# Performance work log

Hardware: AMD Instinct MI355X
Metric: run time of the kernel (lower is better)

The kernel has to match this reference:

```python
import jax, jax.numpy as jnp
import numpy as np
from jax import lax

B, P, C = 2, 512, 5                 # images, proposals/img, classes (incl. background)
IN_FEAT, REP = 12544, 1024          # 256*7*7 pooled features; TwoMLPHead width
H_IMG = W_IMG = 800.0
SCORE_THRESH, NMS_THRESH, DET_PER_IMG = 0.05, 0.5, 100
MIN_SIZE = 0.01
WX, WY, WW, WH = 10.0, 10.0, 5.0, 5.0
BBOX_CLIP = float(np.log(1000.0 / 16.0))
NEG = -1e9


def _make_boxes(key, n):
    k1, k2, k3, k4 = jax.random.split(key, 4)
    cx = jax.random.uniform(k1, (n,)) * W_IMG
    cy = jax.random.uniform(k2, (n,)) * H_IMG
    bw = jax.random.uniform(k3, (n,)) * 180.0 + 20.0
    bh = jax.random.uniform(k4, (n,)) * 180.0 + 20.0
    x1 = jnp.clip(cx - bw / 2, 0.0, W_IMG)
    y1 = jnp.clip(cy - bh / 2, 0.0, H_IMG)
    x2 = jnp.clip(cx + bw / 2, 0.0, W_IMG)
    y2 = jnp.clip(cy + bh / 2, 0.0, H_IMG)
    return jnp.stack([x1, y1, x2, y2], -1).astype(jnp.float32)


def setup_inputs() -> dict:
    ks = jax.random.split(jax.random.key(0), 12)
    box_features = jax.random.normal(ks[0], (B * P, IN_FEAT), jnp.float32)
    proposals = jnp.stack([_make_boxes(ks[1 + i], P) for i in range(B)])
    def w(k, shp):
        return (jax.random.normal(k, shp, jnp.float32) / np.sqrt(shp[0])).astype(jnp.float32)
    return {
        'box_features': box_features,
        'proposals': proposals,
        'W1': w(ks[3], (IN_FEAT, REP)), 'b1': jnp.zeros((REP,), jnp.float32),
        'W2': w(ks[4], (REP, REP)),     'b2': jnp.zeros((REP,), jnp.float32),
        'Wc': w(ks[5], (REP, C)),       'bc': jnp.zeros((C,), jnp.float32),
        'Wb': w(ks[6], (REP, 4 * C)),   'bb': jnp.zeros((4 * C,), jnp.float32),
    }


def box_iou(a, b):
    area_a = (a[:, 2] - a[:, 0]) * (a[:, 3] - a[:, 1])
    area_b = (b[:, 2] - b[:, 0]) * (b[:, 3] - b[:, 1])
    lt = jnp.maximum(a[:, None, :2], b[None, :, :2])
    rb = jnp.minimum(a[:, None, 2:], b[None, :, 2:])
    wh = jnp.clip(rb - lt, 0.0)
    inter = wh[..., 0] * wh[..., 1]
    return inter / (area_a[:, None] + area_b[None, :] - inter + 1e-9)


def decode(reg, props):
    # reg: [N, C, 4] raw deltas; props: [N, 4] xyxy  (torchvision BoxCoder.decode)
    w = props[:, 2] - props[:, 0]
    h = props[:, 3] - props[:, 1]
    cx = props[:, 0] + 0.5 * w
    cy = props[:, 1] + 0.5 * h
    dx, dy = reg[..., 0] / WX, reg[..., 1] / WY
    dw = jnp.minimum(reg[..., 2] / WW, BBOX_CLIP)
    dh = jnp.minimum(reg[..., 3] / WH, BBOX_CLIP)
    pcx = dx * w[:, None] + cx[:, None]
    pcy = dy * h[:, None] + cy[:, None]
    pw = jnp.exp(dw) * w[:, None]
    ph = jnp.exp(dh) * h[:, None]
    return jnp.stack([pcx - 0.5 * pw, pcy - 0.5 * ph, pcx + 0.5 * pw, pcy + 0.5 * ph], -1)


def postprocess_one(boxes, scores, labels):
    # boxes [M,4] (already clipped), scores [M], labels [M] int; fixed-size output.
    M = boxes.shape[0]
    ws = boxes[:, 2] - boxes[:, 0]
    hs = boxes[:, 3] - boxes[:, 1]
    valid = (scores > SCORE_THRESH) & (ws >= MIN_SIZE) & (hs >= MIN_SIZE)
    order = jnp.argsort(-scores)
    b, s, l, v = boxes[order], scores[order], labels[order], valid[order]
    # batched (per-class) NMS via class-offset trick
    off = l.astype(b.dtype)[:, None] * (max(H_IMG, W_IMG) + 1.0)
    iou = box_iou(b + off, b + off)
    idxs = jnp.arange(M)

    def body(i, keep):
        sup = (iou[i] > NMS_THRESH) & keep[i] & (idxs > i)
        return keep & ~sup

    keep = lax.fori_loop(0, M, body, v)
    sc = jnp.where(keep, s, NEG)
    top_s, top_i = lax.top_k(sc, DET_PER_IMG)
    ok = top_s > NEG / 2
    tb = jnp.where(ok[:, None], b[top_i], 0.0)
    tl = jnp.where(ok, l[top_i], 0)
    ts = jnp.where(ok, top_s, 0.0)
    return tb, ts, tl


def reference(box_features, proposals, W1, b1, W2, b2, Wc, bc, Wb, bb):
    # box_head: TwoMLPHead
    h = jax.nn.relu(box_features @ W1 + b1)
    h = jax.nn.relu(h @ W2 + b2)
    # box_predictor
    class_logits = h @ Wc + bc                       # [N, C]
    box_regression = (h @ Wb + bb).reshape(-1, C, 4)  # [N, C, 4]
    props = proposals.reshape(-1, 4)
    pred = decode(box_regression, props)             # [N, C, 4]
    # clip to image
    pred = jnp.stack([
        jnp.clip(pred[..., 0], 0.0, W_IMG), jnp.clip(pred[..., 1], 0.0, H_IMG),
        jnp.clip(pred[..., 2], 0.0, W_IMG), jnp.clip(pred[..., 3], 0.0, H_IMG)], -1)
    scores = jax.nn.softmax(class_logits, -1)        # [N, C]
    # drop background class, flatten proposal-major (matches torch reshape(-1,4))
    pb = pred[:, 1:, :].reshape(B, P * (C - 1), 4)
    sc = scores[:, 1:].reshape(B, P * (C - 1))
    labels = jnp.tile(jnp.arange(1, C, dtype=jnp.int32), P)  # [M]
    boxes_o, scores_o, labels_o = jax.vmap(postprocess_one, in_axes=(0, 0, None))(pb, sc, labels)
    return boxes_o, scores_o, labels_o
```

## Files before the change

kernel.cpp:

```cpp
#include <hip/hip_runtime.h>
#include <math.h>

#define NROWS 1024
#define K1    12544
#define REP   1024
#define NDET  2048
#define DETS  100
#define BBOX_CLIP_F 4.135166556742356f

typedef __attribute__((ext_vector_type(8))) short bf16x8;
typedef __attribute__((ext_vector_type(4))) float f32x4;

__device__ __forceinline__ unsigned short rne_bf16(float x) {
  unsigned u = __float_as_uint(x);
  u += 0x7fffu + ((u >> 16) & 1u);
  return (unsigned short)(u >> 16);
}
__device__ __forceinline__ float bf16f(unsigned short h) {
  return __uint_as_float(((unsigned)h) << 16);
}
__device__ __forceinline__ int swz(int r, int s) {
  return s ^ (r & 3) ^ ((r >> 2) & 3);
}
__device__ __forceinline__ void gload16(const void* g, void* lds) {
  __builtin_amdgcn_global_load_lds(
      (const __attribute__((address_space(1))) unsigned int*)g,
      (__attribute__((address_space(3))) unsigned int*)lds, 16, 0, 0);
}

__global__ __launch_bounds__(256) void pack_fused(
    const float* __restrict__ X, const float* __restrict__ W1,
    const float* __restrict__ W2, const float* __restrict__ Wc,
    const float* __restrict__ Wb,
    unsigned short* __restrict__ Ahp, unsigned short* __restrict__ Alp,
    unsigned short* __restrict__ W1h, unsigned short* __restrict__ W1l,
    unsigned short* __restrict__ W2h, unsigned short* __restrict__ W2l,
    float* __restrict__ Wt) {
  __shared__ unsigned short th[32 * 36], tl[32 * 36];
  const int id = blockIdx.x;
  const int t = threadIdx.x;
  if (id < 13568) {
    const float* W;
    unsigned short *Oh, *Ol;
    int nKB, kb, n0;
    if (id < 12544) { W = W1; Oh = W1h; Ol = W1l; nKB = 392; kb = id % 392; n0 = (id / 392) * 32; }
    else { const int r2 = id - 12544; W = W2; Oh = W2h; Ol = W2l; nKB = 32; kb = r2 % 32; n0 = (r2 / 32) * 32; }
    const int r = t >> 3, c4 = (t & 7) << 2;
    float4 v = *(const float4*)&W[(size_t)(kb * 32 + r) * REP + n0 + c4];
    float fv[4] = {v.x, v.y, v.z, v.w};
#pragma unroll
    for (int j = 0; j < 4; ++j) {
      unsigned short h = rne_bf16(fv[j]);
      th[(c4 + j) * 36 + r] = h;
      tl[(c4 + j) * 36 + r] = rne_bf16(fv[j] - bf16f(h));
    }
    __syncthreads();
    const int half = t >> 7;
    const int n_loc = (t & 127) >> 2, slot = t & 3;
    const unsigned short* src = (half ? tl : th) + n_loc * 36 + slot * 8;
    ushort4 u0 = *(const ushort4*)src;
    ushort4 u1 = *(const ushort4*)(src + 4);
    const int n = n0 + n_loc, rb = n >> 7, rr = n & 127;
    size_t chunk = ((size_t)(rb * nKB + kb)) * 512 + rr * 4 + swz(rr, slot);
    unsigned short* dst = (half ? Ol : Oh) + chunk * 8;
    *(ushort4*)dst = u0;
    *(ushort4*)(dst + 4) = u1;
  } else if (id < 19840) {
    const int r_ = id - 13568;
    const int kb = r_ % 392;
    const int row = (r_ / 392) * 64 + (t >> 2);
    const int slot = t & 3;
    const float* p = X + (size_t)row * K1 + kb * 32 + slot * 8;
    float4 f0 = *(const float4*)p;
    float4 f1 = *(const float4*)(p + 4);
    float fv[8] = {f0.x, f0.y, f0.z, f0.w, f1.x, f1.y, f1.z, f1.w};
    unsigned short hh[8], ll[8];
#pragma unroll
    for (int j = 0; j < 8; ++j) {
      hh[j] = rne_bf16(fv[j]);
      ll[j] = rne_bf16(fv[j] - bf16f(hh[j]));
    }
    const int rb = row >> 7, rr = row & 127;
    size_t chunk = ((size_t)(rb * 392 + kb)) * 512 + rr * 4 + swz(rr, slot);
    unsigned short* dh = Ahp + chunk * 8;
    unsigned short* dl = Alp + chunk * 8;
    *(ushort4*)dh = make_ushort4(hh[0], hh[1], hh[2], hh[3]);
    *(ushort4*)(dh + 4) = make_ushort4(hh[4], hh[5], hh[6], hh[7]);
    *(ushort4*)dl = make_ushort4(ll[0], ll[1], ll[2], ll[3]);
    *(ushort4*)(dl + 4) = make_ushort4(ll[4], ll[5], ll[6], ll[7]);
  } else {
    const int i = (id - 19840) * 256 + t;
    if (i < 25 * 1024) {
      const int o = i >> 10, k = i & 1023;
      Wt[i] = (o < 5) ? Wc[(size_t)k * 5 + o] : Wb[(size_t)k * 20 + (o - 5)];
    }
  }
}

__global__ __launch_bounds__(256) void pack_b(
    const float* __restrict__ W, unsigned short* __restrict__ Oh,
    unsigned short* __restrict__ Ol, int nKB) {
  __shared__ unsigned short th[32 * 36], tl[32 * 36];
  const int kb = blockIdx.x, n0 = blockIdx.y * 32;
  const int t = threadIdx.x;
  const int r = t >> 3, c4 = (t & 7) << 2;
  float4 v = *(const float4*)&W[(size_t)(kb * 32 + r) * REP + n0 + c4];
  float fv[4] = {v.x, v.y, v.z, v.w};
#pragma unroll
  for (int j = 0; j < 4; ++j) {
    unsigned short h = rne_bf16(fv[j]);
    th[(c4 + j) * 36 + r] = h;
    tl[(c4 + j) * 36 + r] = rne_bf16(fv[j] - bf16f(h));
  }
  __syncthreads();
  const int half = t >> 7;
  const int n_loc = (t & 127) >> 2, slot = t & 3;
  const unsigned short* src = (half ? tl : th) + n_loc * 36 + slot * 8;
  ushort4 u0 = *(const ushort4*)src;
  ushort4 u1 = *(const ushort4*)(src + 4);
  const int n = n0 + n_loc, rb = n >> 7, rr = n & 127;
  size_t chunk = ((size_t)(rb * nKB + kb)) * 512 + rr * 4 + swz(rr, slot);
  unsigned short* dst = (half ? Ol : Oh) + chunk * 8;
  *(ushort4*)dst = u0;
  *(ushort4*)(dst + 4) = u1;
}

__global__ __launch_bounds__(256) void gemm_pk2(
    const unsigned short* __restrict__ Ah, const unsigned short* __restrict__ Al,
    const unsigned short* __restrict__ Bh, const unsigned short* __restrict__ Bl,
    float* __restrict__ T, int nKB, int stepsPerZ) {
  __shared__ __align__(16) unsigned short lds[2][4][4096];
  const int tid = threadIdx.x;
  const int w = tid >> 6, l = tid & 63;
  const int r_ = blockIdx.x, t_ = blockIdx.y;
  const int rbA = (r_ & 3) * 2 + (t_ & 1);
  const int rbB = (r_ >> 2) * 4 + (t_ >> 1);
  const int tk0 = blockIdx.z * stepsPerZ;
  const int fr = l & 15, q = l >> 4;
  const int wr = (w >> 1) * 64, wc = (w & 1) * 64;
  const int qs = q ^ (fr & 3) ^ (fr >> 2);
  const int aoff = ((wr + fr) * 4 + qs) * 16;
  const int boff = ((wc + fr) * 4 + qs) * 16;

  auto stage = [&](int bf, int tk) {
    const unsigned short* ga_h = Ah + ((size_t)(rbA * nKB + tk)) * 4096;
    const unsigned short* ga_l = Al + ((size_t)(rbA * nKB + tk)) * 4096;
    const unsigned short* gb_h = Bh + ((size_t)(rbB * nKB + tk)) * 4096;
    const unsigned short* gb_l = Bl + ((size_t)(rbB * nKB + tk)) * 4096;
#pragma unroll
    for (int rseg = 0; rseg < 2; ++rseg) {
      const int seg = rseg * 4 + w;
      const size_t go = (size_t)(seg * 64 + l) * 8;
      gload16(ga_h + go, &lds[bf][0][seg * 512]);
      gload16(ga_l + go, &lds[bf][1][seg * 512]);
      gload16(gb_h + go, &lds[bf][2][seg * 512]);
      gload16(gb_l + go, &lds[bf][3][seg * 512]);
    }
  };

  f32x4 acc[4][4];
#pragma unroll
  for (int m = 0; m < 4; ++m)
#pragma unroll
    for (int n = 0; n < 4; ++n) acc[m][n] = (f32x4){0.f, 0.f, 0.f, 0.f};

  stage(0, tk0);
  if (stepsPerZ > 1) {
    stage(1, tk0 + 1);
    asm volatile("s_waitcnt vmcnt(8)");
  } else {
    asm volatile("s_waitcnt vmcnt(0)");
  }
  __builtin_amdgcn_s_barrier();
  __builtin_amdgcn_sched_barrier(0);

  int cur = 0;
  for (int s = 0; s < stepsPerZ; ++s) {
    const char* La  = (const char*)&lds[cur][0][0];
    const char* Ll  = (const char*)&lds[cur][1][0];
    const char* Lbh = (const char*)&lds[cur][2][0];
    const char* Lbl = (const char*)&lds[cur][3][0];
    bf16x8 ah[4], al[4], bh[4], bl[4];
#pragma unroll
    for (int m = 0; m < 4; ++m) {
      ah[m] = *(const bf16x8*)(La + aoff + m * 1024);
      al[m] = *(const bf16x8*)(Ll + aoff + m * 1024);
    }
#pragma unroll
    for (int n = 0; n < 4; ++n) {
      bh[n] = *(const bf16x8*)(Lbh + boff + n * 1024);
      bl[n] = *(const bf16x8*)(Lbl + boff + n * 1024);
    }
#pragma unroll
    for (int m = 0; m < 4; ++m)
#pragma unroll
      for (int n = 0; n < 4; ++n) {
        acc[m][n] = __builtin_amdgcn_mfma_f32_16x16x32_bf16(ah[m], bh[n], acc[m][n], 0, 0, 0);
        acc[m][n] = __builtin_amdgcn_mfma_f32_16x16x32_bf16(ah[m], bl[n], acc[m][n], 0, 0, 0);
        acc[m][n] = __builtin_amdgcn_mfma_f32_16x16x32_bf16(al[m], bh[n], acc[m][n], 0, 0, 0);
      }
    if (s + 1 < stepsPerZ) {
      __builtin_amdgcn_s_barrier();
      if (s + 2 < stepsPerZ) {
        stage(cur, tk0 + s + 2);
        asm volatile("s_waitcnt vmcnt(8)");
      } else {
        asm volatile("s_waitcnt vmcnt(0)");
      }
      __builtin_amdgcn_s_barrier();
      __builtin_amdgcn_sched_barrier(0);
    }
    cur ^= 1;
  }
  float* Tz = T + (size_t)blockIdx.z * (NROWS * REP);
#pragma unroll
  for (int m = 0; m < 4; ++m) {
    const int r0 = rbA * 128 + wr + m * 16 + ((l >> 4) << 2);
#pragma unroll
    for (int n = 0; n < 4; ++n) {
      const int c = rbB * 128 + wc + n * 16 + fr;
#pragma unroll
      for (int j = 0; j < 4; ++j) Tz[(size_t)(r0 + j) * REP + c] = acc[m][n][j];
    }
  }
}

__global__ __launch_bounds__(256) void combine8_relu_pack(
    const float* __restrict__ T, const float* __restrict__ bias,
    unsigned short* __restrict__ Oh, unsigned short* __restrict__ Ol) {
  const int e = (blockIdx.x * 256 + threadIdx.x) * 8;
  const int MN = NROWS * REP;
  float s[8];
  {
    float4 a0 = *(const float4*)&T[e];
    float4 a1 = *(const float4*)&T[e + 4];
    s[0] = a0.x; s[1] = a0.y; s[2] = a0.z; s[3] = a0.w;
    s[4] = a1.x; s[5] = a1.y; s[6] = a1.z; s[7] = a1.w;
  }
#pragma unroll
  for (int z = 1; z < 8; ++z) {
    float4 a0 = *(const float4*)&T[z * MN + e];
    float4 a1 = *(const float4*)&T[z * MN + e + 4];
    s[0] += a0.x; s[1] += a0.y; s[2] += a0.z; s[3] += a0.w;
    s[4] += a1.x; s[5] += a1.y; s[6] += a1.z; s[7] += a1.w;
  }
  const int c0 = e & 1023;
  float4 b0 = *(const float4*)&bias[c0];
  float4 b1 = *(const float4*)&bias[c0 + 4];
  s[0] = fmaxf(s[0] + b0.x, 0.f); s[1] = fmaxf(s[1] + b0.y, 0.f);
  s[2] = fmaxf(s[2] + b0.z, 0.f); s[3] = fmaxf(s[3] + b0.w, 0.f);
  s[4] = fmaxf(s[4] + b1.x, 0.f); s[5] = fmaxf(s[5] + b1.y, 0.f);
  s[6] = fmaxf(s[6] + b1.z, 0.f); s[7] = fmaxf(s[7] + b1.w, 0.f);
  unsigned short hh[8], ll[8];
#pragma unroll
  for (int j = 0; j < 8; ++j) {
    hh[j] = rne_bf16(s[j]);
    ll[j] = rne_bf16(s[j] - bf16f(hh[j]));
  }
  const int r = e >> 10;
  const int kb = c0 >> 5, slot = (c0 >> 3) & 3;
  const int rb = r >> 7, rr = r & 127;
  size_t chunk = ((size_t)(rb * 32 + kb)) * 512 + rr * 4 + swz(rr, slot);
  unsigned short* dh = Oh + chunk * 8;
  unsigned short* dl = Ol + chunk * 8;
  *(ushort4*)dh = make_ushort4(hh[0], hh[1], hh[2], hh[3]);
  *(ushort4*)(dh + 4) = make_ushort4(hh[4], hh[5], hh[6], hh[7]);
  *(ushort4*)dl = make_ushort4(ll[0], ll[1], ll[2], ll[3]);
  *(ushort4*)(dl + 4) = make_ushort4(ll[4], ll[5], ll[6], ll[7]);
}

__global__ __launch_bounds__(256) void combineN_relu(
    const float* __restrict__ T, const float* __restrict__ bias,
    float* __restrict__ H, int nz) {
  const int i = blockIdx.x * 256 + threadIdx.x;
  const int MN4 = NROWS * REP / 4;
  const float4* t = (const float4*)T;
  float4 s0 = t[i];
  for (int z = 1; z < nz; ++z) {
    float4 v = t[i + z * MN4];
    s0.x += v.x; s0.y += v.y; s0.z += v.z; s0.w += v.w;
  }
  float4 bs = ((const float4*)bias)[i & 255];
  float4 r;
  r.x = fmaxf(s0.x + bs.x, 0.f);
  r.y = fmaxf(s0.y + bs.y, 0.f);
  r.z = fmaxf(s0.z + bs.z, 0.f);
  r.w = fmaxf(s0.w + bs.w, 0.f);
  ((float4*)H)[i] = r;
}

__global__ __launch_bounds__(256) void gemm_pk(
    const float* __restrict__ A, const unsigned short* __restrict__ Bh,
    const unsigned short* __restrict__ Bl, float* __restrict__ T,
    int K, int nKB, int stepsPerZ) {
  __shared__ __align__(16) unsigned short lds[2][4][4096];
  const int tid = threadIdx.x;
  const int w = tid >> 6, l = tid & 63;
  const int bm = blockIdx.x * 128;
  const int bnb = blockIdx.y;
  const int tk0 = blockIdx.z * stepsPerZ;
  const int arow = tid >> 1, ahalf = tid & 1;
  const int fr = l & 15, q = l >> 4;
  const int wr = (w >> 1) * 64, wc = (w & 1) * 64;
  const int qs = q ^ (fr & 3) ^ (fr >> 2);
  const int aoff = ((wr + fr) * 4 + qs) * 16;
  const int boff = ((wc + fr) * 4 + qs) * 16;
  const float* aptr = A + (size_t)(bm + arow) * K + ahalf * 16;

  float4 av[4];
  auto loadA = [&](int tk) {
    const float* p = aptr + tk * 32;
#pragma unroll
    for (int j = 0; j < 4; ++j) av[j] = *(const float4*)(p + j * 4);
  };
  auto stageB = [&](int bf, int tk) {
    const unsigned short* gh = Bh + ((size_t)(bnb * nKB + tk)) * 4096;
    const unsigned short* gl_ = Bl + ((size_t)(bnb * nKB + tk)) * 4096;
#pragma unroll
    for (int rseg = 0; rseg < 2; ++rseg) {
      const int seg = rseg * 4 + w;
      gload16(gh + (size_t)(seg * 64 + l) * 8, &lds[bf][2][seg * 512]);
      gload16(gl_ + (size_t)(seg * 64 + l) * 8, &lds[bf][3][seg * 512]);
    }
  };
  auto writeA = [&](int bf) {
#pragma unroll
    for (int j = 0; j < 2; ++j) {
      const int s_ = ahalf * 2 + j;
      float fv[8] = {av[j * 2].x, av[j * 2].y, av[j * 2].z, av[j * 2].w,
                     av[j * 2 + 1].x, av[j * 2 + 1].y, av[j * 2 + 1].z, av[j * 2 + 1].w};
      unsigned hp[4], lp[4];
#pragma unroll
      for (int p2 = 0; p2 < 4; ++p2) {
        unsigned short h0 = rne_bf16(fv[2 * p2]), h1 = rne_bf16(fv[2 * p2 + 1]);
        float l0 = fv[2 * p2] - bf16f(h0), l1 = fv[2 * p2 + 1] - bf16f(h1);
        hp[p2] = (unsigned)h0 | ((unsigned)h1 << 16);
        lp[p2] = (unsigned)rne_bf16(l0) | ((unsigned)rne_bf16(l1) << 16);
      }
      const int chunk = arow * 4 + swz(arow, s_);
      *(uint4*)&lds[bf][0][chunk * 8] = make_uint4(hp[0], hp[1], hp[2], hp[3]);
      *(uint4*)&lds[bf][1][chunk * 8] = make_uint4(lp[0], lp[1], lp[2], lp[3]);
    }
  };

  f32x4 acc[4][4];
#pragma unroll
  for (int m = 0; m < 4; ++m)
#pragma unroll
    for (int n = 0; n < 4; ++n) acc[m][n] = (f32x4){0.f, 0.f, 0.f, 0.f};

  loadA(tk0);
  stageB(0, tk0);
  writeA(0);
  __syncthreads();
  int cur = 0;
  for (int s = 0; s < stepsPerZ; ++s) {
    const bool nx = (s + 1 < stepsPerZ);
    if (nx) { loadA(tk0 + s + 1); stageB(cur ^ 1, tk0 + s + 1); }
    const char* La = (const char*)&lds[cur][0][0];
    const char* Ll = (const char*)&lds[cur][1][0];
    const char* Lbh = (const char*)&lds[cur][2][0];
    const char* Lbl = (const char*)&lds[cur][3][0];
    bf16x8 ah[4], al[4], bh[4], bl[4];
#pragma unroll
    for (int m = 0; m < 4; ++m) {
      ah[m] = *(const bf16x8*)(La + aoff + m * 1024);
      al[m] = *(const bf16x8*)(Ll + aoff + m * 1024);
    }
#pragma unroll
    for (int n = 0; n < 4; ++n) {
      bh[n] = *(const bf16x8*)(Lbh + boff + n * 1024);
      bl[n] = *(const bf16x8*)(Lbl + boff + n * 1024);
    }
#pragma unroll
    for (int m = 0; m < 4; ++m)
#pragma unroll
      for (int n = 0; n < 4; ++n) {
        acc[m][n] = __builtin_amdgcn_mfma_f32_16x16x32_bf16(ah[m], bh[n], acc[m][n], 0, 0, 0);
        acc[m][n] = __builtin_amdgcn_mfma_f32_16x16x32_bf16(ah[m], bl[n], acc[m][n], 0, 0, 0);
        acc[m][n] = __builtin_amdgcn_mfma_f32_16x16x32_bf16(al[m], bh[n], acc[m][n], 0, 0, 0);
      }
    if (nx) writeA(cur ^ 1);
    __syncthreads();
    cur ^= 1;
  }
  float* Tz = T + (size_t)blockIdx.z * (NROWS * REP);
#pragma unroll
  for (int m = 0; m < 4; ++m) {
    const int r0 = bm + wr + m * 16 + ((l >> 4) << 2);
#pragma unroll
    for (int n = 0; n < 4; ++n) {
      const int c = bnb * 128 + wc + n * 16 + fr;
#pragma unroll
      for (int j = 0; j < 4; ++j) Tz[(size_t)(r0 + j) * REP + c] = acc[m][n][j];
    }
  }
}

__global__ __launch_bounds__(256) void gemm64(
    const float* __restrict__ A, const float* __restrict__ W,
    float* __restrict__ T, int K, int N, int kChunk) {
  __shared__ float As[32][68];
  __shared__ float Bs[32][64];
  const int tid = threadIdx.x;
  const int bm = blockIdx.x * 64, bn = blockIdx.y * 64;
  const int k0 = blockIdx.z * kChunk;
  const int tx = tid & 15, ty = tid >> 4;
  const int ar = tid >> 3;
  const int ac = (tid & 7) << 2;
  const int br = tid >> 4;
  const int bc = (tid & 15) << 2;
  float acc[4][4] = {{0.f,0.f,0.f,0.f},{0.f,0.f,0.f,0.f},{0.f,0.f,0.f,0.f},{0.f,0.f,0.f,0.f}};
  for (int kk = k0; kk < k0 + kChunk; kk += 32) {
    float4 a0 = *(const float4*)&A[(size_t)(bm + ar) * K + kk + ac];
    float4 a1 = *(const float4*)&A[(size_t)(bm + ar + 32) * K + kk + ac];
    float4 b0 = *(const float4*)&W[(size_t)(kk + br) * N + bn + bc];
    float4 b1 = *(const float4*)&W[(size_t)(kk + br + 16) * N + bn + bc];
    As[ac+0][ar] = a0.x; As[ac+1][ar] = a0.y; As[ac+2][ar] = a0.z; As[ac+3][ar] = a0.w;
    As[ac+0][ar+32] = a1.x; As[ac+1][ar+32] = a1.y; As[ac+2][ar+32] = a1.z; As[ac+3][ar+32] = a1.w;
    *(float4*)&Bs[br][bc]    = b0;
    *(float4*)&Bs[br+16][bc] = b1;
    __syncthreads();
#pragma unroll
    for (int k = 0; k < 32; ++k) {
      float4 av = *(const float4*)&As[k][ty << 2];
      float4 bv = *(const float4*)&Bs[k][tx << 2];
      float a_[4] = {av.x, av.y, av.z, av.w};
      float b_[4] = {bv.x, bv.y, bv.z, bv.w};
#pragma unroll
      for (int i = 0; i < 4; ++i)
#pragma unroll
        for (int j = 0; j < 4; ++j)
          acc[i][j] = fmaf(a_[i], b_[j], acc[i][j]);
    }
    __syncthreads();
  }
  float* Tz = T + (size_t)blockIdx.z * NROWS * REP;
#pragma unroll
  for (int i = 0; i < 4; ++i) {
    float4 v = make_float4(acc[i][0], acc[i][1], acc[i][2], acc[i][3]);
    *(float4*)&Tz[(size_t)(bm + (ty << 2) + i) * N + bn + (tx << 2)] = v;
  }
}

__global__ __launch_bounds__(256) void heads2(
    const float* __restrict__ H2, const float* __restrict__ Wt,
    const float* __restrict__ bcv, const float* __restrict__ bbv,
    const float* __restrict__ props, float* __restrict__ pb, float* __restrict__ sc) {
  const int wave = threadIdx.x >> 6, l = threadIdx.x & 63;
  const int n = blockIdx.x * 4 + wave;
  const float* h = H2 + (size_t)n * REP + l * 16;
  float4 h0 = *(const float4*)h, h1 = *(const float4*)(h + 4);
  float4 h2v = *(const float4*)(h + 8), h3 = *(const float4*)(h + 12);
  float outv[25];
#pragma unroll
  for (int o = 0; o < 25; ++o) {
    const float* wp = Wt + o * REP + l * 16;
    float4 w0 = *(const float4*)wp, w1 = *(const float4*)(wp + 4);
    float4 w2 = *(const float4*)(wp + 8), w3 = *(const float4*)(wp + 12);
    float d = h0.x * w0.x;
    d = fmaf(h0.y, w0.y, d); d = fmaf(h0.z, w0.z, d); d = fmaf(h0.w, w0.w, d);
    d = fmaf(h1.x, w1.x, d); d = fmaf(h1.y, w1.y, d); d = fmaf(h1.z, w1.z, d); d = fmaf(h1.w, w1.w, d);
    d = fmaf(h2v.x, w2.x, d); d = fmaf(h2v.y, w2.y, d); d = fmaf(h2v.z, w2.z, d); d = fmaf(h2v.w, w2.w, d);
    d = fmaf(h3.x, w3.x, d); d = fmaf(h3.y, w3.y, d); d = fmaf(h3.z, w3.z, d); d = fmaf(h3.w, w3.w, d);
#pragma unroll
    for (int m = 1; m < 64; m <<= 1) d += __shfl_xor(d, m);
    outv[o] = d + ((o < 5) ? bcv[o] : bbv[o - 5]);
  }
  const float mx = fmaxf(fmaxf(fmaxf(outv[0], outv[1]), fmaxf(outv[2], outv[3])), outv[4]);
  const float e0 = expf(outv[0] - mx), e1 = expf(outv[1] - mx), e2 = expf(outv[2] - mx);
  const float e3 = expf(outv[3] - mx), e4 = expf(outv[4] - mx);
  const float inv = 1.0f / (e0 + e1 + e2 + e3 + e4);
  const float s1 = e1 * inv, s2 = e2 * inv, s3 = e3 * inv, s4 = e4 * inv;
  const float* pr = props + (size_t)n * 4;
  const float x1 = pr[0], y1 = pr[1], x2 = pr[2], y2 = pr[3];
  const float bw = x2 - x1, bh = y2 - y1;
  const float cx = x1 + 0.5f * bw, cy = y1 + 0.5f * bh;
  const int img = n >> 9, pbase = (n & 511) << 2;
#pragma unroll
  for (int c = 1; c <= 4; ++c) {
    if (l == c - 1) {
      const float r0 = outv[5 + c * 4 + 0], r1 = outv[5 + c * 4 + 1];
      const float r2 = outv[5 + c * 4 + 2], r3 = outv[5 + c * 4 + 3];
      const float dx = r0 / 10.0f, dy = r1 / 10.0f;
      const float dw = fminf(r2 / 5.0f, BBOX_CLIP_F);
      const float dh = fminf(r3 / 5.0f, BBOX_CLIP_F);
      const float pcx = dx * bw + cx, pcy = dy * bh + cy;
      const float pw = expf(dw) * bw, ph = expf(dh) * bh;
      float bx1 = pcx - 0.5f * pw, by1 = pcy - 0.5f * ph;
      float bx2 = pcx + 0.5f * pw, by2 = pcy + 0.5f * ph;
      bx1 = fminf(fmaxf(bx1, 0.f), 800.f);
      by1 = fminf(fmaxf(by1, 0.f), 800.f);
      bx2 = fminf(fmaxf(bx2, 0.f), 800.f);
      by2 = fminf(fmaxf(by2, 0.f), 800.f);
      const int pidx = pbase + (c - 1);
      float* o = pb + (size_t)(img * NDET + pidx) * 4;
      o[0] = bx1; o[1] = by1; o[2] = bx2; o[3] = by2;
      const float smc = (c == 1) ? s1 : (c == 2) ? s2 : (c == 3) ? s3 : s4;
      sc[img * NDET + pidx] = smc;
    }
  }
}

__global__ __launch_bounds__(256) void heads_kernel(
    const float* __restrict__ H2, const float* __restrict__ Wc, const float* __restrict__ bcv,
    const float* __restrict__ Wb, const float* __restrict__ bbv,
    const float* __restrict__ props, float* __restrict__ pb, float* __restrict__ sc) {
  const int n = blockIdx.x;
  __shared__ float hrow[REP];
  __shared__ float part[25][8];
  __shared__ float outv[25];
  __shared__ float smax[5];
  const int tid = threadIdx.x;
  ((float4*)hrow)[tid] = ((const float4*)(H2 + (size_t)n * REP))[tid];
  __syncthreads();
  if (tid < 200) {
    const int o = tid >> 3, s = tid & 7;
    float a = 0.f;
    if (o < 5) {
      const float* w = Wc + o;
      for (int k = s * 128; k < s * 128 + 128; ++k) a = fmaf(hrow[k], w[(size_t)k * 5], a);
    } else {
      const float* w = Wb + (o - 5);
      for (int k = s * 128; k < s * 128 + 128; ++k) a = fmaf(hrow[k], w[(size_t)k * 20], a);
    }
    part[o][s] = a;
  }
  __syncthreads();
  if (tid < 25) {
    float a = ((part[tid][0] + part[tid][1]) + (part[tid][2] + part[tid][3]))
            + ((part[tid][4] + part[tid][5]) + (part[tid][6] + part[tid][7]));
    a += (tid < 5) ? bcv[tid] : bbv[tid - 5];
    outv[tid] = a;
  }
  __syncthreads();
  if (tid == 0) {
    float m = outv[0];
    for (int c = 1; c < 5; ++c) m = fmaxf(m, outv[c]);
    float e[5], ssum = 0.f;
    for (int c = 0; c < 5; ++c) { e[c] = expf(outv[c] - m); ssum += e[c]; }
    for (int c = 0; c < 5; ++c) smax[c] = e[c] / ssum;
  }
  __syncthreads();
  if (tid < 4) {
    const int c = tid + 1;
    const float* pr = props + (size_t)n * 4;
    const float x1 = pr[0], y1 = pr[1], x2 = pr[2], y2 = pr[3];
    const float w = x2 - x1, h = y2 - y1;
    const float cx = x1 + 0.5f * w, cy = y1 + 0.5f * h;
    const float r0 = outv[5 + c * 4 + 0], r1 = outv[5 + c * 4 + 1];
    const float r2 = outv[5 + c * 4 + 2], r3 = outv[5 + c * 4 + 3];
    const float dx = r0 / 10.0f, dy = r1 / 10.0f;
    const float dw = fminf(r2 / 5.0f, BBOX_CLIP_F);
    const float dh = fminf(r3 / 5.0f, BBOX_CLIP_F);
    const float pcx = dx * w + cx, pcy = dy * h + cy;
    const float pw = expf(dw) * w, ph = expf(dh) * h;
    float bx1 = pcx - 0.5f * pw, by1 = pcy - 0.5f * ph;
    float bx2 = pcx + 0.5f * pw, by2 = pcy + 0.5f * ph;
    bx1 = fminf(fmaxf(bx1, 0.f), 800.f);
    by1 = fminf(fmaxf(by1, 0.f), 800.f);
    bx2 = fminf(fmaxf(bx2, 0.f), 800.f);
    by2 = fminf(fmaxf(by2, 0.f), 800.f);
    const int img = n >> 9;
    const int pidx = ((n & 511) << 2) + (c - 1);
    float* o = pb + (size_t)(img * NDET + pidx) * 4;
    o[0] = bx1; o[1] = by1; o[2] = bx2; o[3] = by2;
    sc[img * NDET + pidx] = smax[c];
  }
}

__global__ __launch_bounds__(1024) void sortprep_kernel(
    const float* __restrict__ sc, const float* __restrict__ pb,
    float* __restrict__ sbox, float* __restrict__ soff, float* __restrict__ sscore,
    float* __restrict__ sarea, float* __restrict__ slab, unsigned* __restrict__ vword) {
  const int b = blockIdx.x;
  __shared__ unsigned long long key[NDET];
  const int tid = threadIdx.x;
  for (int t = tid; t < NDET; t += 1024) {
    unsigned bits = __float_as_uint(sc[b * NDET + t]);
    key[t] = ((unsigned long long)bits << 32) | (unsigned)(~t);
  }
  __syncthreads();
  for (int k = 2; k <= NDET; k <<= 1) {
    for (int j = k >> 1; j > 0; j >>= 1) {
      for (int t = tid; t < NDET; t += 1024) {
        const int ixj = t ^ j;
        if (ixj > t) {
          const bool up = (t & k) == 0;
          unsigned long long a = key[t], bb_ = key[ixj];
          if ((a < bb_) == up) { key[t] = bb_; key[ixj] = a; }
        }
      }
      __syncthreads();
    }
  }
  for (int pass = 0; pass < 2; ++pass) {
    const int i = pass * 1024 + tid;
    const unsigned oi = ~(unsigned)key[i];
    const float* bx = pb + (size_t)(b * NDET + oi) * 4;
    const float x1 = bx[0], y1 = bx[1], x2 = bx[2], y2 = bx[3];
    const float s = sc[b * NDET + oi];
    const float lab = (float)((oi & 3) + 1);
    const bool valid = (s > 0.05f) && ((x2 - x1) >= 0.01f) && ((y2 - y1) >= 0.01f);
    const float off = lab * 801.0f;
    float* sb = sbox + (size_t)(b * NDET + i) * 4;
    sb[0] = x1; sb[1] = y1; sb[2] = x2; sb[3] = y2;
    float* so = soff + (size_t)(b * NDET + i) * 4;
    so[0] = x1 + off; so[1] = y1 + off; so[2] = x2 + off; so[3] = y2 + off;
    sscore[b * NDET + i] = s;
    sarea[b * NDET + i] = (x2 - x1) * (y2 - y1);
    slab[b * NDET + i] = lab;
    const unsigned long long bal = __ballot(valid);
    if ((i & 31) == 0) vword[b * 64 + (i >> 5)] = (unsigned)(bal >> (i & 32));
  }
}

__global__ __launch_bounds__(256) void mask_kernel(
    const float* __restrict__ soff, const float* __restrict__ sarea,
    unsigned* __restrict__ mask) {
  const int b = blockIdx.y;
  __shared__ float xx1[NDET + 64], yy1[NDET + 64], xx2[NDET + 64], yy2[NDET + 64];
  __shared__ float ar[NDET + 64];
  const int tid = threadIdx.x;
  for (int t = tid; t < NDET; t += 256) {
    float4 v = *(const float4*)(soff + ((size_t)b * NDET + t) * 4);
    const int pt = t + (t >> 5);
    xx1[pt] = v.x; yy1[pt] = v.y; xx2[pt] = v.z; yy2[pt] = v.w;
    ar[pt] = sarea[b * NDET + t];
  }
  __syncthreads();
  const int li = tid >> 6;
  const int w  = tid & 63;
#pragma unroll
  for (int pass = 0; pass < 4; ++pass) {
    const int i = blockIdx.x * 16 + pass * 4 + li;
    const int pi = i + (i >> 5);
    const float ax1 = xx1[pi], ay1 = yy1[pi], ax2 = xx2[pi], ay2 = yy2[pi];
    const float aa = ar[pi];
    unsigned bits = 0;
#pragma unroll 4
    for (int bb = 0; bb < 32; ++bb) {
      const int j = w * 32 + bb;
      const int pj = w * 33 + bb;
      const float ix = fmaxf(fminf(ax2, xx2[pj]) - fmaxf(ax1, xx1[pj]), 0.f);
      const float iy = fmaxf(fminf(ay2, yy2[pj]) - fmaxf(ay1, yy1[pj]), 0.f);
      const float inter = ix * iy;
      const float iou = inter / (aa + ar[pj] - inter + 1e-9f);
      if (j > i && iou > 0.5f) bits |= (1u << bb);
    }
    mask[((size_t)b * NDET + i) * 64 + w] = bits;
  }
}

__global__ __launch_bounds__(64) void scan_kernel(
    const unsigned* __restrict__ vword, const unsigned* __restrict__ mask,
    const float* __restrict__ sbox, const float* __restrict__ sscore,
    const float* __restrict__ slab, float* __restrict__ out) {
  const int b = blockIdx.x;
  const int lane = threadIdx.x;
  unsigned supreg = ~vword[b * 64 + lane];
  __shared__ unsigned short klist[DETS];
  int kcnt = 0;
  for (int w = 0; w < 64 && kcnt < DETS; ++w) {
    unsigned avail = ~__shfl(supreg, w);
    while (avail) {
      const int bb = __ffs(avail) - 1;
      const int i = w * 32 + bb;
      if (lane == 0) klist[kcnt] = (unsigned short)i;
      kcnt++;
      if (kcnt == DETS) break;
      supreg |= mask[((size_t)b * NDET + i) * 64 + lane];
      avail = ~__shfl(supreg, w) & (0xFFFFFFFEu << bb);
    }
  }
  __syncthreads();
  for (int s = lane; s < DETS; s += 64) {
    float b0 = 0.f, b1 = 0.f, b2 = 0.f, b3 = 0.f, sv = 0.f, lv = 0.f;
    if (s < kcnt) {
      const int i = klist[s];
      const float* bx = sbox + ((size_t)b * NDET + i) * 4;
      b0 = bx[0]; b1 = bx[1]; b2 = bx[2]; b3 = bx[3];
      sv = sscore[b * NDET + i];
      lv = slab[b * NDET + i];
    }
    float* ob = out + ((size_t)b * DETS + s) * 4;
    ob[0] = b0; ob[1] = b1; ob[2] = b2; ob[3] = b3;
    out[2 * DETS * 4 + b * DETS + s] = sv;
    out[2 * DETS * 4 + 2 * DETS + b * DETS + s] = lv;
  }
}

extern "C" void kernel_launch(void* const* d_in, const int* in_sizes, int n_in,
                              void* d_out, int out_size, void* d_ws, size_t ws_size,
                              hipStream_t stream) {
  const float* X     = (const float*)d_in[0];
  const float* props = (const float*)d_in[1];
  const float* W1    = (const float*)d_in[2];
  const float* b1    = (const float*)d_in[3];
  const float* W2    = (const float*)d_in[4];
  const float* b2    = (const float*)d_in[5];
  const float* Wc    = (const float*)d_in[6];
  const float* bc    = (const float*)d_in[7];
  const float* Wb    = (const float*)d_in[8];
  const float* bb    = (const float*)d_in[9];
  float* out = (float*)d_out;

  const size_t POST_B = 3200000;
  const size_t NEED_BIG =
      (size_t)9 * 1048576 * 4 +
      (size_t)4 * (size_t)K1 * 1024 * 2 +
      (size_t)4 * 1048576 * 2 + POST_B;
  const size_t NEED_MID =
      (size_t)10 * 1048576 * 4 +
      (size_t)2 * (size_t)K1 * 1024 * 2 +
      (size_t)2 * 1048576 * 2 + 2500000;

  float *T, *H1 = nullptr, *H2, *pb, *sc, *Wt = nullptr;
  unsigned short *W1h = nullptr, *W1l = nullptr, *W2h = nullptr, *W2l = nullptr;
  unsigned short *Ahp = nullptr, *Alp = nullptr, *H1h = nullptr, *H1l = nullptr;
  const int path = (ws_size >= NEED_BIG) ? 2 : (ws_size >= NEED_MID) ? 1 : 0;
  if (path == 2) {
    T   = (float*)d_ws;
    H2  = T + 8 * 1048576;
    W1h = (unsigned short*)(H2 + 1048576);
    W1l = W1h + (size_t)K1 * 1024;
    W2h = W1l + (size_t)K1 * 1024;
    W2l = W2h + 1048576;
    Ahp = W2l + 1048576;
    Alp = Ahp + (size_t)K1 * 1024;
    H1h = Alp + (size_t)K1 * 1024;
    H1l = H1h + 1048576;
    Wt  = (float*)(H1l + 1048576);
    pb  = Wt + 25 * 1024;
  } else if (path == 1) {
    T   = (float*)d_ws;
    H1  = T + 8 * 1048576;
    H2  = H1 + 1048576;
    W1h = (unsigned short*)(H2 + 1048576);
    W1l = W1h + (size_t)K1 * 1024;
    W2h = W1l + (size_t)K1 * 1024;
    W2l = W2h + 1048576;
    pb  = (float*)(W2l + 1048576);
  } else {
    T  = (float*)d_ws;
    H1 = T + 4 * 1048576;
    H2 = H1 + 1048576;
    pb = H2 + 1048576;
  }
  sc = pb + 2 * NDET * 4;
  unsigned* sidx = (unsigned*)(sc + 2 * NDET);
  float* sbox   = (float*)(sidx + 2 * NDET);
  float* soff   = sbox + 2 * NDET * 4;
  float* sscore = soff + 2 * NDET * 4;
  float* sarea  = sscore + 2 * NDET;
  float* slab   = sarea + 2 * NDET;
  unsigned* vword = (unsigned*)(slab + 2 * NDET);
  unsigned* mask  = vword + 128;

  if (path == 2) {
    pack_fused<<<19940, 256, 0, stream>>>(X, W1, W2, Wc, Wb,
                                          Ahp, Alp, W1h, W1l, W2h, W2l, Wt);
    gemm_pk2<<<dim3(8, 8, 8), 256, 0, stream>>>(Ahp, Alp, W1h, W1l, T, K1 / 32, 49);
    combine8_relu_pack<<<512, 256, 0, stream>>>(T, b1, H1h, H1l);
    gemm_pk2<<<dim3(8, 8, 4), 256, 0, stream>>>(H1h, H1l, W2h, W2l, T, 32, 8);
    combineN_relu<<<1024, 256, 0, stream>>>(T, b2, H2, 4);
    heads2<<<256, 256, 0, stream>>>(H2, Wt, bc, bb, props, pb, sc);
  } else if (path == 1) {
    pack_b<<<dim3(K1 / 32, 32), 256, 0, stream>>>(W1, W1h, W1l, K1 / 32);
    pack_b<<<dim3(32, 32), 256, 0, stream>>>(W2, W2h, W2l, 32);
    gemm_pk<<<dim3(8, 8, 8), 256, 0, stream>>>(X, W1h, W1l, T, K1, K1 / 32, 49);
    combineN_relu<<<1024, 256, 0, stream>>>(T, b1, H1, 8);
    gemm_pk<<<dim3(8, 8, 4), 256, 0, stream>>>(H1, W2h, W2l, T, REP, 32, 8);
    combineN_relu<<<1024, 256, 0, stream>>>(T, b2, H2, 4);
    heads_kernel<<<1024, 256, 0, stream>>>(H2, Wc, bc, Wb, bb, props, pb, sc);
  } else {
    gemm64<<<dim3(16, 16, 4), 256, 0, stream>>>(X, W1, T, K1, REP, K1 / 4);
    combineN_relu<<<1024, 256, 0, stream>>>(T, b1, H1, 4);
    gemm64<<<dim3(16, 16, 4), 256, 0, stream>>>(H1, W2, T, REP, REP, REP / 4);
    combineN_relu<<<1024, 256, 0, stream>>>(T, b2, H2, 4);
    heads_kernel<<<1024, 256, 0, stream>>>(H2, Wc, bc, Wb, bb, props, pb, sc);
  }
  sortprep_kernel<<<2, 1024, 0, stream>>>(sc, pb, sbox, soff, sscore, sarea, slab, vword);
  mask_kernel<<<dim3(128, 2), 256, 0, stream>>>(soff, sarea, mask);
  scan_kernel<<<2, 64, 0, stream>>>(vword, mask, sbox, sscore, slab, out);
}
```

Before: 219.4 us.

## Enlarge gemm_pk2 block tile to 256x128 to raise operand reuse

```diff
diff --git a/kernel.cpp b/kernel.cpp
--- a/kernel.cpp
+++ b/kernel.cpp
@@ -125,49 +125,51 @@
   *(ushort4*)(dst + 4) = u1;
 }
 
-__global__ __launch_bounds__(256) void gemm_pk2(
+__global__ __launch_bounds__(256, 1) void gemm_pk2(
     const unsigned short* __restrict__ Ah, const unsigned short* __restrict__ Al,
     const unsigned short* __restrict__ Bh, const unsigned short* __restrict__ Bl,
     float* __restrict__ T, int nKB, int stepsPerZ) {
-  __shared__ __align__(16) unsigned short lds[2][4][4096];
+  __shared__ __align__(16) unsigned short lds[2][6][4096];
   const int tid = threadIdx.x;
   const int w = tid >> 6, l = tid & 63;
-  const int r_ = blockIdx.x, t_ = blockIdx.y;
-  const int rbA = (r_ & 3) * 2 + (t_ & 1);
-  const int rbB = (r_ >> 2) * 4 + (t_ >> 1);
+  const int r_ = blockIdx.x, s_ = blockIdx.y;
+  const int rbA = (r_ & 1) * 2 + (s_ & 1);
+  const int rbB = (r_ >> 1) * 2 + (s_ >> 1);
   const int tk0 = blockIdx.z * stepsPerZ;
   const int fr = l & 15, q = l >> 4;
-  const int wr = (w >> 1) * 64, wc = (w & 1) * 64;
+  const int wt = w >> 1;
+  const int wc = (w & 1) * 64;
   const int qs = q ^ (fr & 3) ^ (fr >> 2);
-  const int aoff = ((wr + fr) * 4 + qs) * 16;
+  const int aoff = (fr * 4 + qs) * 16;
   const int boff = ((wc + fr) * 4 + qs) * 16;
 
   auto stage = [&](int bf, int tk) {
-    const unsigned short* ga_h = Ah + ((size_t)(rbA * nKB + tk)) * 4096;
-    const unsigned short* ga_l = Al + ((size_t)(rbA * nKB + tk)) * 4096;
-    const unsigned short* gb_h = Bh + ((size_t)(rbB * nKB + tk)) * 4096;
-    const unsigned short* gb_l = Bl + ((size_t)(rbB * nKB + tk)) * 4096;
-#pragma unroll
-    for (int rseg = 0; rseg < 2; ++rseg) {
-      const int seg = rseg * 4 + w;
-      const size_t go = (size_t)(seg * 64 + l) * 8;
-      gload16(ga_h + go, &lds[bf][0][seg * 512]);
-      gload16(ga_l + go, &lds[bf][1][seg * 512]);
-      gload16(gb_h + go, &lds[bf][2][seg * 512]);
-      gload16(gb_l + go, &lds[bf][3][seg * 512]);
-    }
+    const unsigned short* srcs[6] = {
+        Ah + ((size_t)((rbA * 2)     * nKB + tk)) * 4096,
+        Ah + ((size_t)((rbA * 2 + 1) * nKB + tk)) * 4096,
+        Al + ((size_t)((rbA * 2)     * nKB + tk)) * 4096,
+        Al + ((size_t)((rbA * 2 + 1) * nKB + tk)) * 4096,
+        Bh + ((size_t)(rbB * nKB + tk)) * 4096,
+        Bl + ((size_t)(rbB * nKB + tk)) * 4096};
+#pragma unroll
+    for (int t6 = 0; t6 < 6; ++t6)
+#pragma unroll
+      for (int rseg = 0; rseg < 2; ++rseg) {
+        const int chunk = rseg * 256 + tid;
+        gload16(srcs[t6] + (size_t)chunk * 8, &lds[bf][t6][(size_t)chunk * 8]);
+      }
   };
 
-  f32x4 acc[4][4];
-#pragma unroll
-  for (int m = 0; m < 4; ++m)
+  f32x4 acc[8][4];
+#pragma unroll
+  for (int m = 0; m < 8; ++m)
 #pragma unroll
     for (int n = 0; n < 4; ++n) acc[m][n] = (f32x4){0.f, 0.f, 0.f, 0.f};
 
   stage(0, tk0);
   if (stepsPerZ > 1) {
     stage(1, tk0 + 1);
-    asm volatile("s_waitcnt vmcnt(8)");
+    asm volatile("s_waitcnt vmcnt(12)");
   } else {
     asm volatile("s_waitcnt vmcnt(0)");
   }
@@ -176,34 +178,32 @@
 
   int cur = 0;
   for (int s = 0; s < stepsPerZ; ++s) {
-    const char* La  = (const char*)&lds[cur][0][0];
-    const char* Ll  = (const char*)&lds[cur][1][0];
-    const char* Lbh = (const char*)&lds[cur][2][0];
-    const char* Lbl = (const char*)&lds[cur][3][0];
-    bf16x8 ah[4], al[4], bh[4], bl[4];
-#pragma unroll
-    for (int m = 0; m < 4; ++m) {
-      ah[m] = *(const bf16x8*)(La + aoff + m * 1024);
-      al[m] = *(const bf16x8*)(Ll + aoff + m * 1024);
-    }
+    const char* LaH = (const char*)&lds[cur][wt][0];
+    const char* LaL = (const char*)&lds[cur][2 + wt][0];
+    const char* Lbh = (const char*)&lds[cur][4][0];
+    const char* Lbl = (const char*)&lds[cur][5][0];
+    bf16x8 bh[4], bl[4];
 #pragma unroll
     for (int n = 0; n < 4; ++n) {
       bh[n] = *(const bf16x8*)(Lbh + boff + n * 1024);
       bl[n] = *(const bf16x8*)(Lbl + boff + n * 1024);
     }
 #pragma unroll
-    for (int m = 0; m < 4; ++m)
+    for (int m = 0; m < 8; ++m) {
+      bf16x8 ahm = *(const bf16x8*)(LaH + aoff + m * 1024);
+      bf16x8 alm = *(const bf16x8*)(LaL + aoff + m * 1024);
 #pragma unroll
       for (int n = 0; n < 4; ++n) {
-        acc[m][n] = __builtin_amdgcn_mfma_f32_16x16x32_bf16(ah[m], bh[n], acc[m][n], 0, 0, 0);
-        acc[m][n] = __builtin_amdgcn_mfma_f32_16x16x32_bf16(ah[m], bl[n], acc[m][n], 0, 0, 0);
-        acc[m][n] = __builtin_amdgcn_mfma_f32_16x16x32_bf16(al[m], bh[n], acc[m][n], 0, 0, 0);
+        acc[m][n] = __builtin_amdgcn_mfma_f32_16x16x32_bf16(ahm, bh[n], acc[m][n], 0, 0, 0);
+        acc[m][n] = __builtin_amdgcn_mfma_f32_16x16x32_bf16(ahm, bl[n], acc[m][n], 0, 0, 0);
+        acc[m][n] = __builtin_amdgcn_mfma_f32_16x16x32_bf16(alm, bh[n], acc[m][n], 0, 0, 0);
       }
+    }
     if (s + 1 < stepsPerZ) {
       __builtin_amdgcn_s_barrier();
       if (s + 2 < stepsPerZ) {
         stage(cur, tk0 + s + 2);
-        asm volatile("s_waitcnt vmcnt(8)");
+        asm volatile("s_waitcnt vmcnt(12)");
       } else {
         asm volatile("s_waitcnt vmcnt(0)");
       }
@@ -214,8 +214,8 @@
   }
   float* Tz = T + (size_t)blockIdx.z * (NROWS * REP);
 #pragma unroll
-  for (int m = 0; m < 4; ++m) {
-    const int r0 = rbA * 128 + wr + m * 16 + ((l >> 4) << 2);
+  for (int m = 0; m < 8; ++m) {
+    const int r0 = rbA * 256 + wt * 128 + m * 16 + ((l >> 4) << 2);
 #pragma unroll
     for (int n = 0; n < 4; ++n) {
       const int c = rbB * 128 + wc + n * 16 + fr;
@@ -760,9 +760,9 @@
   if (path == 2) {
     pack_fused<<<19940, 256, 0, stream>>>(X, W1, W2, Wc, Wb,
                                           Ahp, Alp, W1h, W1l, W2h, W2l, Wt);
-    gemm_pk2<<<dim3(8, 8, 8), 256, 0, stream>>>(Ahp, Alp, W1h, W1l, T, K1 / 32, 49);
+    gemm_pk2<<<dim3(8, 4, 8), 256, 0, stream>>>(Ahp, Alp, W1h, W1l, T, K1 / 32, 49);
     combine8_relu_pack<<<512, 256, 0, stream>>>(T, b1, H1h, H1l);
-    gemm_pk2<<<dim3(8, 8, 4), 256, 0, stream>>>(H1h, H1l, W2h, W2l, T, 32, 8);
+    gemm_pk2<<<dim3(8, 4, 4), 256, 0, stream>>>(H1h, H1l, W2h, W2l, T, 32, 8);
     combineN_relu<<<1024, 256, 0, stream>>>(T, b2, H2, 4);
     heads2<<<256, 256, 0, stream>>>(H2, Wt, bc, bb, props, pb, sc);
   } else if (path == 1) {
```

Measured after the change: 236.4 us. 7.8% more time.
